# Kernel tuning notes

Hardware: AMD Instinct MI355X
Metric: run time of the kernel (lower is better)

The kernel has to match this reference:

```python
import jax, jax.numpy as jnp
import numpy as np

B, S, H = 32, 512, 768          # batch, encoder seq len, hidden size
W, G = 128, 4                   # max words per example, max tokens per word group
NH, HD, FF, NL, NLAB = 4, 192, 2048, 2, 6  # heads, head dim, ffn dim, layers, labels
EPS = 1e-5


def setup_inputs() -> dict:
    key = jax.random.key(0)
    ks = jax.random.split(key, 16)
    s = 0.02
    hidden = jax.random.normal(ks[0], (B, S, H), jnp.float32)
    word_token_idx = jax.random.randint(ks[1], (B, W, G), 0, S).astype(jnp.int32)
    glen = jax.random.randint(ks[2], (B, W), 1, G + 1)
    group_token_mask = jnp.arange(G)[None, None, :] < glen[:, :, None]  # [B,W,G] bool
    nwords = jax.random.randint(ks[3], (B,), W // 2, W + 1)
    word_valid = jnp.arange(W)[None, :] < nwords[:, None]               # [B,W] bool
    return {
        'hidden': hidden,
        'word_token_idx': word_token_idx,
        'group_token_mask': group_token_mask,
        'word_valid': word_valid,
        'qkv_w': jax.random.normal(ks[4], (NL, 3 * H, H), jnp.float32) * s,
        'qkv_b': jnp.zeros((NL, 3 * H), jnp.float32),
        'out_w': jax.random.normal(ks[5], (NL, H, H), jnp.float32) * s,
        'out_b': jnp.zeros((NL, H), jnp.float32),
        'ff1_w': jax.random.normal(ks[6], (NL, FF, H), jnp.float32) * s,
        'ff1_b': jnp.zeros((NL, FF), jnp.float32),
        'ff2_w': jax.random.normal(ks[7], (NL, H, FF), jnp.float32) * s,
        'ff2_b': jnp.zeros((NL, H), jnp.float32),
        'ln1_s': jnp.ones((NL, H), jnp.float32),
        'ln1_b': jnp.zeros((NL, H), jnp.float32),
        'ln2_s': jnp.ones((NL, H), jnp.float32),
        'ln2_b': jnp.zeros((NL, H), jnp.float32),
        'cls_w': jax.random.normal(ks[8], (NLAB, H), jnp.float32) * s,
        'cls_b': jnp.zeros((NLAB,), jnp.float32),
    }


def _ln(x, s, b):
    m = x.mean(-1, keepdims=True)
    v = ((x - m) ** 2).mean(-1, keepdims=True)
    return (x - m) * jax.lax.rsqrt(v + EPS) * s + b


def reference(hidden, word_token_idx, group_token_mask, word_valid,
              qkv_w, qkv_b, out_w, out_b, ff1_w, ff1_b, ff2_w, ff2_b,
              ln1_s, ln1_b, ln2_s, ln2_b, cls_w, cls_b):
    dt = hidden.dtype
    # ragged per-word gather + masked mean over each subword group: [B,W,G,H]
    gathered = jax.vmap(lambda h, i: h[i])(hidden, word_token_idx)
    gm = group_token_mask[..., None].astype(dt)
    wemb = (gathered * gm).sum(2) / jnp.maximum(gm.sum(2), 1.0)   # [B,W,H]
    # invalid (padded) words are zero, matching torch pad_sequence zero-padding
    wemb = wemb * word_valid[..., None].astype(dt)
    cls = hidden[:, 0, :]
    x = jnp.concatenate([cls[:, None, :], wemb], axis=1)          # [B, W+1, H]
    # key padding mask: True = padded position; CLS slot always valid
    pad = jnp.concatenate([jnp.zeros((B, 1), bool), ~word_valid], axis=1)
    neg = jnp.finfo(dt).min
    Lw = W + 1
    scale = 1.0 / np.sqrt(HD)
    for l in range(NL):  # 2 post-norm TransformerEncoder layers
        qkv = x @ qkv_w[l].T + qkv_b[l]
        q, k, v = jnp.split(qkv, 3, axis=-1)
        q = q.reshape(B, Lw, NH, HD).transpose(0, 2, 1, 3)
        k = k.reshape(B, Lw, NH, HD).transpose(0, 2, 1, 3)
        v = v.reshape(B, Lw, NH, HD).transpose(0, 2, 1, 3)
        scores = jnp.einsum('bhqd,bhkd->bhqk', q, k) * scale
        scores = jnp.where(pad[:, None, None, :], neg, scores)
        a = jax.nn.softmax(scores, axis=-1)
        ctx = jnp.einsum('bhqk,bhkd->bhqd', a, v).transpose(0, 2, 1, 3).reshape(B, Lw, H)
        attn = ctx @ out_w[l].T + out_b[l]
        x = _ln(x + attn, ln1_s[l], ln1_b[l])
        h1 = jax.nn.relu(x @ ff1_w[l].T + ff1_b[l])
        x = _ln(x + h1 @ ff2_w[l].T + ff2_b[l], ln2_s[l], ln2_b[l])
    pooled = x[:, 0, :]
    logits = pooled @ cls_w.T + cls_b
    return (logits, pooled)
```

## Files before the change

kernel.cpp:

```cpp
#include <hip/hip_runtime.h>
#include <hip/hip_bf16.h>
#include <math.h>

#define B_  32
#define S_  512
#define H_  768
#define W_  128
#define G_  4
#define LW  129
#define NH_ 4
#define HD_ 192
#define FF_ 2048
#define NL_ 2
#define NLAB_ 6
#define M_   (B_ * LW)
#define MPAD 4224
#define EPS_ 1e-5f
#define SCALE_ 0.07216878364870323f

#define TP 192
#define KP 160
#define KR 144
#define KLD 200
#define PLD 168

#define QW_SZ (3 * H_ * H_)
#define OW_SZ (H_ * H_)
#define F1_SZ (FF_ * H_)
#define F2_SZ (H_ * FF_)
#define WL_SZ (QW_SZ + OW_SZ + F1_SZ + F2_SZ)

typedef __bf16 bf16_8 __attribute__((ext_vector_type(8)));
typedef float  f32x4  __attribute__((ext_vector_type(4)));
typedef unsigned short ushort8_t __attribute__((ext_vector_type(8)));

__device__ __forceinline__ float b2f(unsigned short u) {
    union { unsigned int i; float f; } c; c.i = ((unsigned int)u) << 16; return c.f;
}
__device__ __forceinline__ unsigned short f2b(float f) {
    union { float f; unsigned int u; } c; c.f = f;
    unsigned int u = c.u;
    return (unsigned short)((u + 0x7FFFu + ((u >> 16) & 1u)) >> 16);
}

__device__ __forceinline__ float wave_sum(float v) {
#pragma unroll
    for (int off = 1; off < 64; off <<= 1) v += __shfl_xor(v, off, 64);
    return v;
}
__device__ __forceinline__ float wave_max(float v) {
#pragma unroll
    for (int off = 1; off < 64; off <<= 1) v = fmaxf(v, __shfl_xor(v, off, 64));
    return v;
}
__device__ __forceinline__ float block_sum(float v, float* red) {
    v = wave_sum(v);
    int wid = threadIdx.x >> 6, lane = threadIdx.x & 63;
    if (lane == 0) red[wid] = v;
    __syncthreads();
    float r = (red[0] + red[1]) + (red[2] + red[3]);
    __syncthreads();
    return r;
}

__global__ __launch_bounds__(256) void build_cvt_kernel(
    const float* __restrict__ hidden,
    const int*   __restrict__ wti,
    const int*   __restrict__ gmask,
    const int*   __restrict__ wvalid,
    unsigned short* __restrict__ xb,
    const float4* __restrict__ qw, const float4* __restrict__ ow,
    const float4* __restrict__ f1, const float4* __restrict__ f2,
    ushort4* __restrict__ dst)
{
    int bx = blockIdx.x;
    int tid = threadIdx.x;
    if (bx >= (LW + 3) * B_) {
        constexpr int WL4 = WL_SZ / 4;
        int i = (bx - (LW + 3) * B_) * 256 + tid;
        int l = (i < WL4) ? 0 : 1;
        int j = i - l * WL4;
        float4 v;
        if (j < QW_SZ / 4)                          v = qw[l * (QW_SZ / 4) + j];
        else if (j < (QW_SZ + OW_SZ) / 4)           v = ow[l * (OW_SZ / 4) + j - QW_SZ / 4];
        else if (j < (QW_SZ + OW_SZ + F1_SZ) / 4)   v = f1[l * (F1_SZ / 4) + j - (QW_SZ + OW_SZ) / 4];
        else                                        v = f2[l * (F2_SZ / 4) + j - (QW_SZ + OW_SZ + F1_SZ) / 4];
        ushort4 o; o.x = f2b(v.x); o.y = f2b(v.y); o.z = f2b(v.z); o.w = f2b(v.w);
        dst[i] = o;
        return;
    }
    int t = bx % (LW + 3);
    int b = bx / (LW + 3);
    if (t >= LW) {
        int pr = M_ + b * 3 + (t - LW);
        size_t xo = (size_t)pr * H_;
#pragma unroll
        for (int i = 0; i < 3; i++) xb[xo + tid + i * 256] = 0;
        return;
    }
    size_t xo = ((size_t)b * LW + t) * H_;
    if (t == 0) {
        const float* src = hidden + (size_t)b * S_ * H_;
#pragma unroll
        for (int i = 0; i < 3; i++) xb[xo + tid + i * 256] = f2b(src[tid + i * 256]);
    } else {
        int w = t - 1;
        int valid = wvalid[b * W_ + w];
        int ids[G_]; float msk[G_]; float cnt = 0.f;
#pragma unroll
        for (int g = 0; g < G_; g++) {
            ids[g] = wti[(b * W_ + w) * G_ + g];
            msk[g] = (gmask[(b * W_ + w) * G_ + g] != 0) ? 1.f : 0.f;
            cnt += msk[g];
        }
        float inv = valid ? (1.f / fmaxf(cnt, 1.f)) : 0.f;
#pragma unroll
        for (int i = 0; i < 3; i++) {
            int c = tid + i * 256;
            float a = 0.f;
#pragma unroll
            for (int g = 0; g < G_; g++)
                a += msk[g] * hidden[((size_t)b * S_ + ids[g]) * H_ + c];
            xb[xo + c] = f2b(a * inv);
        }
    }
}

template <int BM, int BN, int BK, int RELU, int OUTBF>
__device__ __forceinline__ void gemm_body(
    unsigned short* As, unsigned short* Bs,
    const unsigned short* __restrict__ A,
    const unsigned short* __restrict__ Bw,
    const float* __restrict__ bias,
    void* __restrict__ Cout,
    int N, int K, int ldc, int lda, int bm, int bn)
{
    constexpr int MI  = BM / 32;
    constexpr int NJ  = BN / 32;
    constexpr int CPR = BK / 8;
    constexpr int RPL = 2048 / BK;
    constexpr int SA  = BM * BK / 2048;
    constexpr int SB  = BN * BK / 2048;

    const int tid  = threadIdx.x;
    const int lane = tid & 63;
    const int wid  = tid >> 6;

    const int wm = (wid & 1) * (BM / 2);
    const int wn = (wid >> 1) * (BN / 2);
    const int r  = lane & 15;
    const int q8 = lane >> 4;
    const int m8 = r & (CPR - 1);

    const int srow = tid / CPR;
    const int scol = (tid % CPR) ^ (srow & (CPR - 1));
    const unsigned short* Ag = A  + (size_t)(bm + srow) * lda + scol * 8;
    const unsigned short* Bg = Bw + (size_t)(bn + srow) * K + scol * 8;

    const bf16_8* Af = (const bf16_8*)As;
    const bf16_8* Bf = (const bf16_8*)Bs;
    int arow[MI], brow[NJ];
#pragma unroll
    for (int i = 0; i < MI; i++) arow[i] = (wm + i * 16 + r) * CPR;
#pragma unroll
    for (int j = 0; j < NJ; j++) brow[j] = (wn + j * 16 + r) * CPR;

    f32x4 acc[MI][NJ];
#pragma unroll
    for (int i = 0; i < MI; i++)
#pragma unroll
        for (int j = 0; j < NJ; j++) acc[i][j] = (f32x4){0.f, 0.f, 0.f, 0.f};

    for (int k0 = 0; k0 < K; k0 += BK) {
#pragma unroll
        for (int s = 0; s < SA; s++)
            __builtin_amdgcn_global_load_lds(
                (const __attribute__((address_space(1))) void*)(Ag + (size_t)(s * RPL) * lda + k0),
                (__attribute__((address_space(3))) void*)(As + s * 2048 + tid * 8), 16, 0, 0);
#pragma unroll
        for (int s = 0; s < SB; s++)
            __builtin_amdgcn_global_load_lds(
                (const __attribute__((address_space(1))) void*)(Bg + (size_t)(s * RPL) * K + k0),
                (__attribute__((address_space(3))) void*)(Bs + s * 2048 + tid * 8), 16, 0, 0);
        __syncthreads();
#pragma unroll
        for (int ks = 0; ks < BK / 32; ks++) {
            const int cc = (ks * 4 + q8) ^ m8;
            bf16_8 a[MI], b[NJ];
#pragma unroll
            for (int i = 0; i < MI; i++) a[i] = Af[arow[i] + cc];
#pragma unroll
            for (int j = 0; j < NJ; j++) b[j] = Bf[brow[j] + cc];
#pragma unroll
            for (int i = 0; i < MI; i++)
#pragma unroll
                for (int j = 0; j < NJ; j++)
                    acc[i][j] = __builtin_amdgcn_mfma_f32_16x16x32_bf16(a[i], b[j], acc[i][j], 0, 0, 0);
        }
        __syncthreads();
    }

    int col[NJ]; float bv[NJ];
#pragma unroll
    for (int j = 0; j < NJ; j++) { col[j] = bn + wn + j * 16 + r; bv[j] = bias[col[j]]; }
    const int row0 = bm + wm + ((lane >> 4) << 2);
#pragma unroll
    for (int i = 0; i < MI; i++) {
#pragma unroll
        for (int rg = 0; rg < 4; rg++) {
            size_t rowoff = (size_t)(row0 + i * 16 + rg) * ldc;
#pragma unroll
            for (int j = 0; j < NJ; j++) {
                float v = acc[i][j][rg] + bv[j];
                if (RELU) v = fmaxf(v, 0.f);
                if (OUTBF) ((unsigned short*)Cout)[rowoff + col[j]] = f2b(v);
                else       ((float*)Cout)[rowoff + col[j]] = v;
            }
        }
    }
}

template <int BM, int BN, int BK, int RELU, int OUTBF, int SWZ>
__global__ __launch_bounds__(256) void gemm_mfma(
    const unsigned short* __restrict__ A,
    const unsigned short* __restrict__ Bw,
    const float* __restrict__ bias,
    void* __restrict__ Cout,
    int N, int K, int ldc, int lda)
{
    __shared__ __align__(16) unsigned short As[BM * BK];
    __shared__ __align__(16) unsigned short Bs[BN * BK];
    int bx = blockIdx.x, by = blockIdx.y;
    if (SWZ) {
        int nx = gridDim.x;
        int total = nx * gridDim.y;
        int id = by * nx + bx;
        int id2 = (id & 7) * (total >> 3) + (id >> 3);
        by = id2 / nx; bx = id2 - by * nx;
    }
    gemm_body<BM, BN, BK, RELU, OUTBF>(As, Bs, A, Bw, bias, Cout, N, K, ldc, lda,
                                       by * BM, bx * BN);
}

__global__ __launch_bounds__(256) void gemm_kv_q_kernel(
    const unsigned short* __restrict__ xb,
    const unsigned short* __restrict__ wkv,
    const float* __restrict__ bkv,
    unsigned short* __restrict__ kvout,
    const unsigned short* __restrict__ wq,
    const float* __restrict__ qb,
    unsigned short* __restrict__ qrows)
{
    __shared__ __align__(16) unsigned short As[64 * 64];
    __shared__ __align__(16) unsigned short Bs[128 * 64];
    int bx = blockIdx.x, by = blockIdx.y;
    if (bx == 12) {
        if (by >= 6) return;
        gemm_body<64, 128, 64, 0, 1>(As, Bs, xb, wq, qb, qrows,
                                     H_, H_, H_, LW * H_, 0, by * 128);
        return;
    }
    int id = by * 12 + bx;
    int id2 = (id & 7) * (792 >> 3) + (id >> 3);
    by = id2 / 12; bx = id2 - by * 12;
    gemm_body<64, 128, 64, 0, 1>(As, Bs, xb, wkv, bkv, kvout,
                                 2 * H_, H_, 3 * H_, H_, by * 64, bx * 128);
}

__global__ __launch_bounds__(256) void vt_kernel(
    const unsigned short* __restrict__ qkv,
    unsigned short* __restrict__ vtb)
{
    __shared__ __align__(16) unsigned short Vs[KR * KLD];
    int bh = blockIdx.x;
    int b = bh >> 2, h = bh & 3;
    int tid = threadIdx.x;
    for (int c = tid; c < KR * 24; c += 256) {
        int t = c / 24, j = c - t * 24;
        ushort8_t v = (ushort8_t){0,0,0,0,0,0,0,0};
        if (t < LW)
            v = *(const ushort8_t*)(qkv + (size_t)(b * LW + t) * (3 * H_) + 2 * H_ + h * HD_ + j * 8);
        *(ushort8_t*)(&Vs[t * KLD + j * 8]) = v;
    }
    __syncthreads();
    size_t obase = (size_t)bh * (HD_ * KP);
    for (int c = tid; c < HD_ * (KP / 4); c += 256) {
        int d = c / (KP / 4), t0 = (c - d * (KP / 4)) * 4;
        ushort4 o;
        o.x = (t0 + 0 < KR) ? Vs[(t0 + 0) * KLD + d] : 0;
        o.y = (t0 + 1 < KR) ? Vs[(t0 + 1) * KLD + d] : 0;
        o.z = (t0 + 2 < KR) ? Vs[(t0 + 2) * KLD + d] : 0;
        o.w = (t0 + 3 < KR) ? Vs[(t0 + 3) * KLD + d] : 0;
        *(ushort4*)(&vtb[obase + (size_t)d * KP + t0]) = o;
    }
}

__global__ __launch_bounds__(256) void attn_fused_kernel(
    const unsigned short* __restrict__ qkv,
    const int*            __restrict__ wvalid,
    const unsigned short* __restrict__ vtb,
    unsigned short*       __restrict__ ctx)
{
    __shared__ __align__(16) unsigned short Ks[KR * KLD];
    __shared__ __align__(16) unsigned short Ps[64 * PLD];
    __shared__ float msk[KR];
    int mb = blockIdx.x;
    int bh = blockIdx.y;
    int b = bh >> 2, h = bh & 3;
    int tid = threadIdx.x, lane = tid & 63, wid = tid >> 6;
    int q = lane >> 4, r = lane & 15;

    for (int c = tid; c < KR * 24; c += 256) {
        int t = c / 24, j = c - t * 24;
        ushort8_t v = (ushort8_t){0,0,0,0,0,0,0,0};
        if (t < LW)
            v = *(const ushort8_t*)(qkv + (size_t)(b * LW + t) * (3 * H_) + H_ + h * HD_ + j * 8);
        *(ushort8_t*)(&Ks[t * KLD + j * 8]) = v;
    }
    if (tid < KR) {
        bool valid = (tid == 0) || (tid <= W_ && wvalid[b * W_ + tid - 1] != 0);
        msk[tid] = valid ? 0.f : -1e30f;
    }
    __syncthreads();

    const int lrow0 = wid * 16;
    const bool p1_active = (mb < 2) || (lrow0 == 0);
    if (p1_active) {
        const unsigned short* Qp = qkv + ((size_t)(b * LW) + mb * 64 + lrow0 + r) * (3 * H_) + h * HD_;
        f32x4 acc[9];
#pragma unroll
        for (int nt = 0; nt < 9; nt++) acc[nt] = (f32x4){0.f, 0.f, 0.f, 0.f};
        for (int ks = 0; ks < HD_ / 32; ks++) {
            bf16_8 a = *(const bf16_8*)(Qp + ks * 32 + q * 8);
#pragma unroll
            for (int nt = 0; nt < 9; nt++) {
                bf16_8 bfrag = *(const bf16_8*)(&Ks[(nt * 16 + r) * KLD + ks * 32 + q * 8]);
                acc[nt] = __builtin_amdgcn_mfma_f32_16x16x32_bf16(a, bfrag, acc[nt], 0, 0, 0);
            }
        }
        float mk[9];
#pragma unroll
        for (int nt = 0; nt < 9; nt++) mk[nt] = msk[nt * 16 + r];
#pragma unroll
        for (int rg = 0; rg < 4; rg++) {
            float v[9]; float mx = -1e30f;
#pragma unroll
            for (int nt = 0; nt < 9; nt++) { v[nt] = acc[nt][rg] * SCALE_ + mk[nt]; mx = fmaxf(mx, v[nt]); }
#pragma unroll
            for (int off = 1; off < 16; off <<= 1) mx = fmaxf(mx, __shfl_xor(mx, off, 64));
            float s = 0.f;
#pragma unroll
            for (int nt = 0; nt < 9; nt++) { v[nt] = __expf(v[nt] - mx); s += v[nt]; }
#pragma unroll
            for (int off = 1; off < 16; off <<= 1) s += __shfl_xor(s, off, 64);
            float inv = 1.f / s;
            int lr = lrow0 + q * 4 + rg;
#pragma unroll
            for (int nt = 0; nt < 9; nt++)
                Ps[lr * PLD + nt * 16 + r] = f2b(v[nt] * inv);
            Ps[lr * PLD + KR + r] = 0;
        }
    }
    __syncthreads();

    const int wm = (wid & 1) * 32, wn = (wid >> 1) * 96;
    if (!(mb == 2 && wm == 32)) {
        size_t vbase = (size_t)bh * (HD_ * KP);
        f32x4 pacc[2][6];
#pragma unroll
        for (int i = 0; i < 2; i++)
#pragma unroll
            for (int j = 0; j < 6; j++) pacc[i][j] = (f32x4){0.f, 0.f, 0.f, 0.f};

        for (int ks = 0; ks < KP / 32; ks++) {
            bf16_8 a[2], bb[6];
#pragma unroll
            for (int i = 0; i < 2; i++)
                a[i] = *(const bf16_8*)(&Ps[(wm + i * 16 + r) * PLD + ks * 32 + q * 8]);
#pragma unroll
            for (int j = 0; j < 6; j++)
                bb[j] = *(const bf16_8*)(vtb + vbase + (size_t)(wn + j * 16 + r) * KP + ks * 32 + q * 8);
#pragma unroll
            for (int i = 0; i < 2; i++)
#pragma unroll
                for (int j = 0; j < 6; j++)
                    pacc[i][j] = __builtin_amdgcn_mfma_f32_16x16x32_bf16(a[i], bb[j], pacc[i][j], 0, 0, 0);
        }

#pragma unroll
        for (int i = 0; i < 2; i++) {
#pragma unroll
            for (int rg = 0; rg < 4; rg++) {
                int tl = mb * 64 + wm + i * 16 + q * 4 + rg;
                if (tl < LW) {
                    size_t rowoff = (size_t)(b * LW + tl) * H_ + h * HD_;
#pragma unroll
                    for (int j = 0; j < 6; j++)
                        ctx[rowoff + wn + j * 16 + r] = f2b(pacc[i][j][rg]);
                }
            }
        }
    }
}

__global__ __launch_bounds__(256) void add_ln_kernel(
    unsigned short* __restrict__ xb, const unsigned short* __restrict__ res,
    const float* __restrict__ sc, const float* __restrict__ bi)
{
    __shared__ float red[4];
    int row = blockIdx.x;
    int tid = threadIdx.x;
    size_t base = (size_t)row * H_;
    float v[3];
    float sum = 0.f;
#pragma unroll
    for (int i = 0; i < 3; i++) {
        int c = tid + i * 256;
        float t = b2f(xb[base + c]) + b2f(res[base + c]);
        v[i] = t; sum += t;
    }
    sum = block_sum(sum, red);
    float mean = sum * (1.f / H_);
    float var = 0.f;
#pragma unroll
    for (int i = 0; i < 3; i++) { float d = v[i] - mean; var += d * d; }
    var = block_sum(var, red);
    float inv = rsqrtf(var * (1.f / H_) + EPS_);
#pragma unroll
    for (int i = 0; i < 3; i++) {
        int c = tid + i * 256;
        xb[base + c] = f2b((v[i] - mean) * inv * sc[c] + bi[c]);
    }
}

__global__ __launch_bounds__(256) void cls_attn_core2_kernel(
    const unsigned short* __restrict__ qrows,
    const unsigned short* __restrict__ qkvb,
    const int* __restrict__ wvalid,
    unsigned short* __restrict__ ctxc)
{
    __shared__ float qh[HD_];
    __shared__ float sr[160];
    __shared__ float ps[LW];
    __shared__ float red[4];
    int b = blockIdx.x, h = blockIdx.y;
    int tid = threadIdx.x, lane = tid & 63, wid = tid >> 6;
    if (tid < HD_) qh[tid] = b2f(qrows[(size_t)b * H_ + h * HD_ + tid]);
    __syncthreads();
    int grp = tid >> 3, s8 = tid & 7;
#pragma unroll
    for (int p = 0; p < 5; p++) {
        int t = p * 32 + grp;
        float acc = 0.f;
        if (t < LW) {
            const unsigned short* kr = qkvb + (size_t)(b * LW + t) * (3 * H_) + H_ + h * HD_ + s8 * 24;
#pragma unroll
            for (int j = 0; j < 3; j++) {
                ushort8_t k8 = *(const ushort8_t*)(kr + j * 8);
#pragma unroll
                for (int jj = 0; jj < 8; jj++) acc += qh[s8 * 24 + j * 8 + jj] * b2f(k8[jj]);
            }
        }
        acc += __shfl_xor(acc, 1, 64);
        acc += __shfl_xor(acc, 2, 64);
        acc += __shfl_xor(acc, 4, 64);
        if (s8 == 0 && t < LW) {
            bool valid = (t == 0) || (wvalid[b * W_ + t - 1] != 0);
            sr[t] = valid ? acc * SCALE_ : -1e30f;
        }
    }
    __syncthreads();
    float sc = (tid < LW) ? sr[tid] : -1e30f;
    float mx = wave_max(sc);
    if (lane == 0) red[wid] = mx;
    __syncthreads();
    mx = fmaxf(fmaxf(red[0], red[1]), fmaxf(red[2], red[3]));
    __syncthreads();
    float e = (tid < LW) ? __expf(sc - mx) : 0.f;
    float ssum = wave_sum(e);
    if (lane == 0) red[wid] = ssum;
    __syncthreads();
    ssum = (red[0] + red[1]) + (red[2] + red[3]);
    if (tid < LW) ps[tid] = e * (1.f / ssum);
    __syncthreads();
    if (tid < HD_) {
        const unsigned short* vb = qkvb + (size_t)(b * LW) * (3 * H_) + 2 * H_ + h * HD_ + tid;
        float cx = 0.f;
#pragma unroll 8
        for (int t = 0; t < LW; t++)
            cx += ps[t] * b2f(vb[(size_t)t * (3 * H_)]);
        ctxc[(size_t)b * H_ + h * HD_ + tid] = f2b(cx);
    }
}

__global__ __launch_bounds__(256) void cls_ln1_kernel(
    const unsigned short* __restrict__ proj,
    const unsigned short* __restrict__ xb,
    const float* __restrict__ sc, const float* __restrict__ bi,
    unsigned short* __restrict__ dst)
{
    __shared__ float red[4];
    int b = blockIdx.x;
    int tid = threadIdx.x;
    float v[3]; float sum = 0.f;
#pragma unroll
    for (int i = 0; i < 3; i++) {
        int c = tid + i * 256;
        float t = b2f(proj[(size_t)b * H_ + c]) + b2f(xb[(size_t)(b * LW) * H_ + c]);
        v[i] = t; sum += t;
    }
    sum = block_sum(sum, red);
    float mean = sum * (1.f / H_);
    float var = 0.f;
#pragma unroll
    for (int i = 0; i < 3; i++) { float d = v[i] - mean; var += d * d; }
    var = block_sum(var, red);
    float inv = rsqrtf(var * (1.f / H_) + EPS_);
#pragma unroll
    for (int i = 0; i < 3; i++) {
        int c = tid + i * 256;
        dst[(size_t)b * H_ + c] = f2b((v[i] - mean) * inv * sc[c] + bi[c]);
    }
}

__global__ __launch_bounds__(256) void cls_final_kernel(
    const unsigned short* __restrict__ proj,
    const unsigned short* __restrict__ resid,
    const float* __restrict__ ln2s, const float* __restrict__ ln2b,
    const float* __restrict__ cls_w, const float* __restrict__ cls_b,
    float* __restrict__ out)
{
    __shared__ float red[4];
    __shared__ float lred[4][NLAB_];
    int b = blockIdx.x;
    int tid = threadIdx.x, lane = tid & 63, wid = tid >> 6;
    size_t base = (size_t)b * H_;
    float v[3]; float sum = 0.f;
#pragma unroll
    for (int i = 0; i < 3; i++) {
        int c = tid + i * 256;
        float t = b2f(proj[base + c]) + b2f(resid[base + c]);
        v[i] = t; sum += t;
    }
    sum = block_sum(sum, red);
    float mean = sum * (1.f / H_);
    float var = 0.f;
#pragma unroll
    for (int i = 0; i < 3; i++) { float d = v[i] - mean; var += d * d; }
    var = block_sum(var, red);
    float rinv = rsqrtf(var * (1.f / H_) + EPS_);
    float f3[3];
#pragma unroll
    for (int i = 0; i < 3; i++) {
        int c = tid + i * 256;
        f3[i] = (v[i] - mean) * rinv * ln2s[c] + ln2b[c];
        out[B_ * NLAB_ + b * H_ + c] = f3[i];
    }
    float l6[NLAB_] = {0.f, 0.f, 0.f, 0.f, 0.f, 0.f};
#pragma unroll
    for (int i = 0; i < 3; i++) {
        int c = tid + i * 256;
#pragma unroll
        for (int w = 0; w < NLAB_; w++) l6[w] += f3[i] * cls_w[w * H_ + c];
    }
#pragma unroll
    for (int w = 0; w < NLAB_; w++) l6[w] = wave_sum(l6[w]);
    if (lane == 0) {
#pragma unroll
        for (int w = 0; w < NLAB_; w++) lred[wid][w] = l6[w];
    }
    __syncthreads();
    if (tid < NLAB_)
        out[b * NLAB_ + tid] = lred[0][tid] + lred[1][tid] + lred[2][tid] + lred[3][tid] + cls_b[tid];
}

extern "C" void kernel_launch(void* const* d_in, const int* in_sizes, int n_in,
                              void* d_out, int out_size, void* d_ws, size_t ws_size,
                              hipStream_t stream) {
    const float* hidden = (const float*)d_in[0];
    const int*   wti    = (const int*)d_in[1];
    const int*   gmask  = (const int*)d_in[2];
    const int*   wvalid = (const int*)d_in[3];
    const float* qkv_w  = (const float*)d_in[4];
    const float* qkv_b  = (const float*)d_in[5];
    const float* out_w  = (const float*)d_in[6];
    const float* out_b  = (const float*)d_in[7];
    const float* ff1_w  = (const float*)d_in[8];
    const float* ff1_b  = (const float*)d_in[9];
    const float* ff2_w  = (const float*)d_in[10];
    const float* ff2_b  = (const float*)d_in[11];
    const float* ln1_s  = (const float*)d_in[12];
    const float* ln1_b  = (const float*)d_in[13];
    const float* ln2_s  = (const float*)d_in[14];
    const float* ln2_b  = (const float*)d_in[15];
    const float* cls_w  = (const float*)d_in[16];
    const float* cls_b  = (const float*)d_in[17];
    float* out = (float*)d_out;

    const size_t XSZ = (size_t)MPAD * H_;
    const size_t ASZ = (size_t)128 * TP * KP;
    const size_t R64 = (size_t)64 * H_;
    unsigned short* U    = (unsigned short*)d_ws;
    unsigned short* vtb  = U;
    unsigned short* tmpb = U;
    unsigned short* qrows64 = U + 1 * R64;
    unsigned short* ctxc  = U + 2 * R64;
    unsigned short* xc64  = U + 3 * R64;
    unsigned short* tmp64 = U + 4 * R64;
    unsigned short* h1c   = U + 5 * R64;
    unsigned short* xb   = U + ASZ;
    unsigned short* ctxb = xb + XSZ;
    unsigned short* qkvb = ctxb + XSZ;
    unsigned short* wb   = qkvb + (size_t)MPAD * 3 * H_;

    build_cvt_kernel<<<(LW + 3) * B_ + 2 * WL_SZ / 4 / 256, 256, 0, stream>>>(
        hidden, wti, gmask, wvalid, xb,
        (const float4*)qkv_w, (const float4*)out_w,
        (const float4*)ff1_w, (const float4*)ff2_w, (ushort4*)wb);

    const int GM = MPAD / 64;

    {
        unsigned short* wbl = wb;
        gemm_mfma<64, 128, 64, 0, 1, 0><<<dim3(3 * H_ / 128, GM), 256, 0, stream>>>(
            xb, wbl, qkv_b, qkvb, 3 * H_, H_, 3 * H_, H_);
        vt_kernel<<<128, 256, 0, stream>>>(qkvb, vtb);
        attn_fused_kernel<<<dim3(3, 128), 256, 0, stream>>>(qkvb, wvalid, vtb, ctxb);
        gemm_mfma<64, 64, 64, 0, 1, 1><<<dim3(H_ / 64, GM), 256, 0, stream>>>(
            ctxb, wbl + QW_SZ, out_b, tmpb, H_, H_, H_, H_);
        add_ln_kernel<<<M_, 256, 0, stream>>>(xb, tmpb, ln1_s, ln1_b);
        gemm_mfma<64, 128, 64, 1, 1, 1><<<dim3(FF_ / 128, GM), 256, 0, stream>>>(
            xb, wbl + QW_SZ + OW_SZ, ff1_b, qkvb, FF_, H_, FF_, H_);
        gemm_mfma<64, 64, 64, 0, 1, 1><<<dim3(H_ / 64, GM), 256, 0, stream>>>(
            qkvb, wbl + QW_SZ + OW_SZ + F1_SZ, ff2_b, tmpb, H_, FF_, H_, FF_);
        add_ln_kernel<<<M_, 256, 0, stream>>>(xb, tmpb, ln2_s, ln2_b);
    }

    {
        unsigned short* wbl = wb + WL_SZ;
        gemm_kv_q_kernel<<<dim3(13, GM), 256, 0, stream>>>(
            xb, wbl + (size_t)H_ * H_, qkv_b + 3 * H_ + H_, qkvb + H_,
            wbl, qkv_b + 3 * H_, qrows64);
        cls_attn_core2_kernel<<<dim3(B_, NH_), 256, 0, stream>>>(
            qrows64, qkvb, wvalid, ctxc);
        gemm_mfma<64, 128, 64, 0, 1, 0><<<dim3(H_ / 128, 1), 256, 0, stream>>>(
            ctxc, wbl + QW_SZ, out_b + H_, tmp64, H_, H_, H_, H_);
        cls_ln1_kernel<<<B_, 256, 0, stream>>>(tmp64, xb, ln1_s + H_, ln1_b + H_, xc64);
        gemm_mfma<64, 128, 64, 1, 1, 0><<<dim3(FF_ / 128, 1), 256, 0, stream>>>(
            xc64, wbl + QW_SZ + OW_SZ, ff1_b + FF_, h1c, FF_, H_, FF_, H_);
        gemm_mfma<64, 128, 64, 0, 1, 0><<<dim3(H_ / 128, 1), 256, 0, stream>>>(
            h1c, wbl + QW_SZ + OW_SZ + F1_SZ, ff2_b + H_, tmp64, H_, FF_, H_, FF_);
        cls_final_kernel<<<B_, 256, 0, stream>>>(tmp64, xc64, ln2_s + H_, ln2_b + H_,
                                                 cls_w, cls_b, out);
    }
    (void)in_sizes; (void)n_in; (void)out_size; (void)ws_size;
}
```

Baseline: 376.6 us.

## Fuse CLS-row tail of last layer into one cooperative kernel

Replaces six small launches for the last layer's CLS-only path (attention core, out-proj GEMM, LN1, FF1, FF2, final LN plus classifier) with a single cooperative kernel of 128 blocks. Phases are separated by grid.sync and reuse a gemm_body device helper. This is meant to remove per-launch overhead and inter-kernel gaps on a latency-bound tail. In exchange it adds grid-wide barriers and leaves most blocks idle in the small GEMM phases.

```diff
diff --git a/kernel.cpp b/kernel.cpp
--- a/kernel.cpp
+++ b/kernel.cpp
@@ -1,6 +1,9 @@
 #include <hip/hip_runtime.h>
 #include <hip/hip_bf16.h>
+#include <hip/hip_cooperative_groups.h>
 #include <math.h>
+
+namespace cg = cooperative_groups;
 
 #define B_  32
 #define S_  512
@@ -75,9 +78,10 @@
 {
     int bx = blockIdx.x;
     int tid = threadIdx.x;
-    if (bx >= (LW + 3) * B_) {
+    constexpr int NGATHER = (LW + 3) * B_;
+    if (bx >= NGATHER) {
         constexpr int WL4 = WL_SZ / 4;
-        int i = (bx - (LW + 3) * B_) * 256 + tid;
+        int i = (bx - NGATHER) * 256 + tid;
         int l = (i < WL4) ? 0 : 1;
         int j = i - l * WL4;
         float4 v;
@@ -433,145 +437,160 @@
     }
 }
 
-__global__ __launch_bounds__(256) void cls_attn_core2_kernel(
+__global__ __launch_bounds__(256) void cls_tail_fused_kernel(
     const unsigned short* __restrict__ qrows,
     const unsigned short* __restrict__ qkvb,
     const int* __restrict__ wvalid,
-    unsigned short* __restrict__ ctxc)
-{
+    const unsigned short* __restrict__ xb,
+    const unsigned short* __restrict__ wo, const float* __restrict__ ob,
+    const float* __restrict__ ln1s, const float* __restrict__ ln1b,
+    const unsigned short* __restrict__ f1w, const float* __restrict__ f1b,
+    const unsigned short* __restrict__ f2w, const float* __restrict__ f2bias,
+    const float* __restrict__ ln2s, const float* __restrict__ ln2b,
+    const float* __restrict__ cls_w, const float* __restrict__ cls_b,
+    unsigned short* __restrict__ ctxc, unsigned short* __restrict__ xc64,
+    unsigned short* __restrict__ tmp64, unsigned short* __restrict__ h1c,
+    float* __restrict__ out)
+{
+    __shared__ __align__(16) unsigned short As[64 * 64];
+    __shared__ __align__(16) unsigned short Bs[128 * 64];
     __shared__ float qh[HD_];
     __shared__ float sr[160];
     __shared__ float ps[LW];
     __shared__ float red[4];
-    int b = blockIdx.x, h = blockIdx.y;
-    int tid = threadIdx.x, lane = tid & 63, wid = tid >> 6;
-    if (tid < HD_) qh[tid] = b2f(qrows[(size_t)b * H_ + h * HD_ + tid]);
-    __syncthreads();
-    int grp = tid >> 3, s8 = tid & 7;
-#pragma unroll
-    for (int p = 0; p < 5; p++) {
-        int t = p * 32 + grp;
-        float acc = 0.f;
-        if (t < LW) {
-            const unsigned short* kr = qkvb + (size_t)(b * LW + t) * (3 * H_) + H_ + h * HD_ + s8 * 24;
-#pragma unroll
-            for (int j = 0; j < 3; j++) {
-                ushort8_t k8 = *(const ushort8_t*)(kr + j * 8);
-#pragma unroll
-                for (int jj = 0; jj < 8; jj++) acc += qh[s8 * 24 + j * 8 + jj] * b2f(k8[jj]);
+    __shared__ float lred[4][NLAB_];
+    cg::grid_group grid = cg::this_grid();
+    const int blk = blockIdx.x;
+    const int tid = threadIdx.x, lane = tid & 63, wid = tid >> 6;
+
+    {
+        int b = blk >> 2, h = blk & 3;
+        if (tid < HD_) qh[tid] = b2f(qrows[(size_t)b * H_ + h * HD_ + tid]);
+        __syncthreads();
+        int grp = tid >> 3, s8 = tid & 7;
+#pragma unroll
+        for (int p = 0; p < 5; p++) {
+            int t = p * 32 + grp;
+            float acc = 0.f;
+            if (t < LW) {
+                const unsigned short* kr = qkvb + (size_t)(b * LW + t) * (3 * H_) + H_ + h * HD_ + s8 * 24;
+#pragma unroll
+                for (int j = 0; j < 3; j++) {
+                    ushort8_t k8 = *(const ushort8_t*)(kr + j * 8);
+#pragma unroll
+                    for (int jj = 0; jj < 8; jj++) acc += qh[s8 * 24 + j * 8 + jj] * b2f(k8[jj]);
+                }
             }
-        }
-        acc += __shfl_xor(acc, 1, 64);
-        acc += __shfl_xor(acc, 2, 64);
-        acc += __shfl_xor(acc, 4, 64);
-        if (s8 == 0 && t < LW) {
-            bool valid = (t == 0) || (wvalid[b * W_ + t - 1] != 0);
-            sr[t] = valid ? acc * SCALE_ : -1e30f;
-        }
-    }
-    __syncthreads();
-    float sc = (tid < LW) ? sr[tid] : -1e30f;
-    float mx = wave_max(sc);
-    if (lane == 0) red[wid] = mx;
-    __syncthreads();
-    mx = fmaxf(fmaxf(red[0], red[1]), fmaxf(red[2], red[3]));
-    __syncthreads();
-    float e = (tid < LW) ? __expf(sc - mx) : 0.f;
-    float ssum = wave_sum(e);
-    if (lane == 0) red[wid] = ssum;
-    __syncthreads();
-    ssum = (red[0] + red[1]) + (red[2] + red[3]);
-    if (tid < LW) ps[tid] = e * (1.f / ssum);
-    __syncthreads();
-    if (tid < HD_) {
-        const unsigned short* vb = qkvb + (size_t)(b * LW) * (3 * H_) + 2 * H_ + h * HD_ + tid;
-        float cx = 0.f;
+            acc += __shfl_xor(acc, 1, 64);
+            acc += __shfl_xor(acc, 2, 64);
+            acc += __shfl_xor(acc, 4, 64);
+            if (s8 == 0 && t < LW) {
+                bool valid = (t == 0) || (wvalid[b * W_ + t - 1] != 0);
+                sr[t] = valid ? acc * SCALE_ : -1e30f;
+            }
+        }
+        __syncthreads();
+        float sc = (tid < LW) ? sr[tid] : -1e30f;
+        float mx = wave_max(sc);
+        if (lane == 0) red[wid] = mx;
+        __syncthreads();
+        mx = fmaxf(fmaxf(red[0], red[1]), fmaxf(red[2], red[3]));
+        __syncthreads();
+        float e = (tid < LW) ? __expf(sc - mx) : 0.f;
+        float ssum = wave_sum(e);
+        if (lane == 0) red[wid] = ssum;
+        __syncthreads();
+        ssum = (red[0] + red[1]) + (red[2] + red[3]);
+        if (tid < LW) ps[tid] = e * (1.f / ssum);
+        __syncthreads();
+        if (tid < HD_) {
+            const unsigned short* vb = qkvb + (size_t)(b * LW) * (3 * H_) + 2 * H_ + h * HD_ + tid;
+            float cx = 0.f;
 #pragma unroll 8
-        for (int t = 0; t < LW; t++)
-            cx += ps[t] * b2f(vb[(size_t)t * (3 * H_)]);
-        ctxc[(size_t)b * H_ + h * HD_ + tid] = f2b(cx);
-    }
-}
-
-__global__ __launch_bounds__(256) void cls_ln1_kernel(
-    const unsigned short* __restrict__ proj,
-    const unsigned short* __restrict__ xb,
-    const float* __restrict__ sc, const float* __restrict__ bi,
-    unsigned short* __restrict__ dst)
-{
-    __shared__ float red[4];
-    int b = blockIdx.x;
-    int tid = threadIdx.x;
-    float v[3]; float sum = 0.f;
-#pragma unroll
-    for (int i = 0; i < 3; i++) {
-        int c = tid + i * 256;
-        float t = b2f(proj[(size_t)b * H_ + c]) + b2f(xb[(size_t)(b * LW) * H_ + c]);
-        v[i] = t; sum += t;
-    }
-    sum = block_sum(sum, red);
-    float mean = sum * (1.f / H_);
-    float var = 0.f;
-#pragma unroll
-    for (int i = 0; i < 3; i++) { float d = v[i] - mean; var += d * d; }
-    var = block_sum(var, red);
-    float inv = rsqrtf(var * (1.f / H_) + EPS_);
-#pragma unroll
-    for (int i = 0; i < 3; i++) {
-        int c = tid + i * 256;
-        dst[(size_t)b * H_ + c] = f2b((v[i] - mean) * inv * sc[c] + bi[c]);
-    }
-}
-
-__global__ __launch_bounds__(256) void cls_final_kernel(
-    const unsigned short* __restrict__ proj,
-    const unsigned short* __restrict__ resid,
-    const float* __restrict__ ln2s, const float* __restrict__ ln2b,
-    const float* __restrict__ cls_w, const float* __restrict__ cls_b,
-    float* __restrict__ out)
-{
-    __shared__ float red[4];
-    __shared__ float lred[4][NLAB_];
-    int b = blockIdx.x;
-    int tid = threadIdx.x, lane = tid & 63, wid = tid >> 6;
-    size_t base = (size_t)b * H_;
-    float v[3]; float sum = 0.f;
-#pragma unroll
-    for (int i = 0; i < 3; i++) {
-        int c = tid + i * 256;
-        float t = b2f(proj[base + c]) + b2f(resid[base + c]);
-        v[i] = t; sum += t;
-    }
-    sum = block_sum(sum, red);
-    float mean = sum * (1.f / H_);
-    float var = 0.f;
-#pragma unroll
-    for (int i = 0; i < 3; i++) { float d = v[i] - mean; var += d * d; }
-    var = block_sum(var, red);
-    float rinv = rsqrtf(var * (1.f / H_) + EPS_);
-    float f3[3];
-#pragma unroll
-    for (int i = 0; i < 3; i++) {
-        int c = tid + i * 256;
-        f3[i] = (v[i] - mean) * rinv * ln2s[c] + ln2b[c];
-        out[B_ * NLAB_ + b * H_ + c] = f3[i];
-    }
-    float l6[NLAB_] = {0.f, 0.f, 0.f, 0.f, 0.f, 0.f};
-#pragma unroll
-    for (int i = 0; i < 3; i++) {
-        int c = tid + i * 256;
-#pragma unroll
-        for (int w = 0; w < NLAB_; w++) l6[w] += f3[i] * cls_w[w * H_ + c];
-    }
-#pragma unroll
-    for (int w = 0; w < NLAB_; w++) l6[w] = wave_sum(l6[w]);
-    if (lane == 0) {
-#pragma unroll
-        for (int w = 0; w < NLAB_; w++) lred[wid][w] = l6[w];
-    }
-    __syncthreads();
-    if (tid < NLAB_)
-        out[b * NLAB_ + tid] = lred[0][tid] + lred[1][tid] + lred[2][tid] + lred[3][tid] + cls_b[tid];
+            for (int t = 0; t < LW; t++)
+                cx += ps[t] * b2f(vb[(size_t)t * (3 * H_)]);
+            ctxc[(size_t)b * H_ + h * HD_ + tid] = f2b(cx);
+        }
+    }
+    grid.sync();
+
+    if (blk < 6)
+        gemm_body<64, 128, 64, 0, 1>(As, Bs, ctxc, wo, ob, tmp64, H_, H_, H_, H_, 0, blk * 128);
+    grid.sync();
+
+    if (blk < B_) {
+        int b = blk;
+        float v[3]; float sum = 0.f;
+#pragma unroll
+        for (int i = 0; i < 3; i++) {
+            int c = tid + i * 256;
+            float t = b2f(tmp64[(size_t)b * H_ + c]) + b2f(xb[(size_t)(b * LW) * H_ + c]);
+            v[i] = t; sum += t;
+        }
+        sum = block_sum(sum, red);
+        float mean = sum * (1.f / H_);
+        float var = 0.f;
+#pragma unroll
+        for (int i = 0; i < 3; i++) { float d = v[i] - mean; var += d * d; }
+        var = block_sum(var, red);
+        float inv = rsqrtf(var * (1.f / H_) + EPS_);
+#pragma unroll
+        for (int i = 0; i < 3; i++) {
+            int c = tid + i * 256;
+            xc64[(size_t)b * H_ + c] = f2b((v[i] - mean) * inv * ln1s[c] + ln1b[c]);
+        }
+    }
+    grid.sync();
+
+    if (blk < 16)
+        gemm_body<64, 128, 64, 1, 1>(As, Bs, xc64, f1w, f1b, h1c, FF_, H_, FF_, H_, 0, blk * 128);
+    grid.sync();
+
+    if (blk < 6)
+        gemm_body<64, 128, 64, 0, 1>(As, Bs, h1c, f2w, f2bias, tmp64, H_, FF_, H_, FF_, 0, blk * 128);
+    grid.sync();
+
+    if (blk < B_) {
+        int b = blk;
+        size_t base = (size_t)b * H_;
+        float v[3]; float sum = 0.f;
+#pragma unroll
+        for (int i = 0; i < 3; i++) {
+            int c = tid + i * 256;
+            float t = b2f(tmp64[base + c]) + b2f(xc64[base + c]);
+            v[i] = t; sum += t;
+        }
+        sum = block_sum(sum, red);
+        float mean = sum * (1.f / H_);
+        float var = 0.f;
+#pragma unroll
+        for (int i = 0; i < 3; i++) { float d = v[i] - mean; var += d * d; }
+        var = block_sum(var, red);
+        float rinv = rsqrtf(var * (1.f / H_) + EPS_);
+        float f3[3];
+#pragma unroll
+        for (int i = 0; i < 3; i++) {
+            int c = tid + i * 256;
+            f3[i] = (v[i] - mean) * rinv * ln2s[c] + ln2b[c];
+            out[B_ * NLAB_ + b * H_ + c] = f3[i];
+        }
+        float l6[NLAB_] = {0.f, 0.f, 0.f, 0.f, 0.f, 0.f};
+#pragma unroll
+        for (int i = 0; i < 3; i++) {
+            int c = tid + i * 256;
+#pragma unroll
+            for (int w = 0; w < NLAB_; w++) l6[w] += f3[i] * cls_w[w * H_ + c];
+        }
+#pragma unroll
+        for (int w = 0; w < NLAB_; w++) l6[w] = wave_sum(l6[w]);
+        if (lane == 0) {
+#pragma unroll
+            for (int w = 0; w < NLAB_; w++) lred[wid][w] = l6[w];
+        }
+        __syncthreads();
+        if (tid < NLAB_)
+            out[b * NLAB_ + tid] = lred[0][tid] + lred[1][tid] + lred[2][tid] + lred[3][tid] + cls_b[tid];
+    }
 }
 
 extern "C" void kernel_launch(void* const* d_in, const int* in_sizes, int n_in,
@@ -641,17 +660,37 @@
         gemm_kv_q_kernel<<<dim3(13, GM), 256, 0, stream>>>(
             xb, wbl + (size_t)H_ * H_, qkv_b + 3 * H_ + H_, qkvb + H_,
             wbl, qkv_b + 3 * H_, qrows64);
-        cls_attn_core2_kernel<<<dim3(B_, NH_), 256, 0, stream>>>(
-            qrows64, qkvb, wvalid, ctxc);
-        gemm_mfma<64, 128, 64, 0, 1, 0><<<dim3(H_ / 128, 1), 256, 0, stream>>>(
-            ctxc, wbl + QW_SZ, out_b + H_, tmp64, H_, H_, H_, H_);
-        cls_ln1_kernel<<<B_, 256, 0, stream>>>(tmp64, xb, ln1_s + H_, ln1_b + H_, xc64);
-        gemm_mfma<64, 128, 64, 1, 1, 0><<<dim3(FF_ / 128, 1), 256, 0, stream>>>(
-            xc64, wbl + QW_SZ + OW_SZ, ff1_b + FF_, h1c, FF_, H_, FF_, H_);
-        gemm_mfma<64, 128, 64, 0, 1, 0><<<dim3(H_ / 128, 1), 256, 0, stream>>>(
-            h1c, wbl + QW_SZ + OW_SZ + F1_SZ, ff2_b + H_, tmp64, H_, FF_, H_, FF_);
-        cls_final_kernel<<<B_, 256, 0, stream>>>(tmp64, xc64, ln2_s + H_, ln2_b + H_,
-                                                 cls_w, cls_b, out);
+        const unsigned short* qrows_a = qrows64;
+        const unsigned short* qkvb_a  = qkvb;
+        const int*            wv_a    = wvalid;
+        const unsigned short* xb_a    = xb;
+        const unsigned short* wo_a    = wbl + QW_SZ;
+        const float*          ob_a    = out_b + H_;
+        const float*          l1s_a   = ln1_s + H_;
+        const float*          l1b_a   = ln1_b + H_;
+        const unsigned short* f1w_a   = wbl + QW_SZ + OW_SZ;
+        const float*          f1b_a   = ff1_b + FF_;
+        const unsigned short* f2w_a   = wbl + QW_SZ + OW_SZ + F1_SZ;
+        const float*          f2b_a   = ff2_b + H_;
+        const float*          l2s_a   = ln2_s + H_;
+        const float*          l2b_a   = ln2_b + H_;
+        const float*          cw_a    = cls_w;
+        const float*          cb_a    = cls_b;
+        unsigned short*       ctxc_a  = ctxc;
+        unsigned short*       xc64_a  = xc64;
+        unsigned short*       tmp64_a = tmp64;
+        unsigned short*       h1c_a   = h1c;
+        float*                out_a   = out;
+        void* kargs[] = {
+            (void*)&qrows_a, (void*)&qkvb_a, (void*)&wv_a, (void*)&xb_a,
+            (void*)&wo_a, (void*)&ob_a, (void*)&l1s_a, (void*)&l1b_a,
+            (void*)&f1w_a, (void*)&f1b_a, (void*)&f2w_a, (void*)&f2b_a,
+            (void*)&l2s_a, (void*)&l2b_a, (void*)&cw_a, (void*)&cb_a,
+            (void*)&ctxc_a, (void*)&xc64_a, (void*)&tmp64_a, (void*)&h1c_a,
+            (void*)&out_a
+        };
+        hipLaunchCooperativeKernel((void*)cls_tail_fused_kernel,
+                                   dim3(128), dim3(256), kargs, 0, stream);
     }
     (void)in_sizes; (void)n_in; (void)out_size; (void)ws_size;
 }
```

Result: slower. 478.3 us (+27.0%).
